# Kernel tuning notes

Hardware: AMD Instinct MI355X
Metric: run time of the kernel (lower is better)

Reference implementation:

```python
import jax, jax.numpy as jnp
import numpy as np

HID = 1024
VOCAB = 50257
MAXLEN = 2048


def setup_inputs() -> dict:
    key = jax.random.key(0)
    ks = jax.random.split(key, 12)
    s = 0.02
    return {
        "input_tok": jax.random.randint(ks[0], (1,), 0, VOCAB),
        "hidden": jax.random.normal(ks[1], (1, 1, HID), jnp.float32),
        "encoder_outputs": jax.random.normal(ks[2], (MAXLEN, HID), jnp.float32),
        "emb": jax.random.normal(ks[3], (VOCAB, HID), jnp.float32) * s,
        "attn_W": jax.random.normal(ks[4], (MAXLEN, 2 * HID), jnp.float32) * s,
        "attn_b": jnp.zeros((MAXLEN,), jnp.float32),
        "comb_W": jax.random.normal(ks[5], (HID, 2 * HID), jnp.float32) * s,
        "comb_b": jnp.zeros((HID,), jnp.float32),
        "W_ih": jax.random.normal(ks[6], (3 * HID, HID), jnp.float32) * s,
        "W_hh": jax.random.normal(ks[7], (3 * HID, HID), jnp.float32) * s,
        "b_ih": jnp.zeros((3 * HID,), jnp.float32),
        "b_hh": jnp.zeros((3 * HID,), jnp.float32),
        "out_W": jax.random.normal(ks[8], (VOCAB, HID), jnp.float32) * s,
        "out_b": jnp.zeros((VOCAB,), jnp.float32),
    }


def reference(input_tok, hidden, encoder_outputs, emb, attn_W, attn_b,
              comb_W, comb_b, W_ih, W_hh, b_ih, b_hh, out_W, out_b):
    H = hidden.shape[-1]
    # embedding lookup -> [1, H]; dropout is identity in eval mode
    embedded = emb[input_tok].reshape(1, H)
    h = hidden[0]  # [1, H]
    # Bahdanau-style attention over fixed max_length
    attn_weights = jax.nn.softmax(
        jnp.concatenate([embedded, h], axis=1) @ attn_W.T + attn_b, axis=1)  # [1, L]
    attn_applied = attn_weights @ encoder_outputs  # [1, H]
    x = jnp.concatenate([embedded, attn_applied], axis=1) @ comb_W.T + comb_b
    x = jax.nn.relu(x)  # [1, H]
    # single GRU step (PyTorch gate layout: r, z, n)
    gi = x @ W_ih.T + b_ih
    gh = h @ W_hh.T + b_hh
    gi_r, gi_z, gi_n = jnp.split(gi, 3, axis=1)
    gh_r, gh_z, gh_n = jnp.split(gh, 3, axis=1)
    r = jax.nn.sigmoid(gi_r + gh_r)
    z = jax.nn.sigmoid(gi_z + gh_z)
    n = jnp.tanh(gi_n + r * gh_n)
    h_new = (1.0 - z) * n + z * h  # [1, H]
    out = jax.nn.log_softmax(h_new @ out_W.T + out_b, axis=1)  # [1, V]
    return out, h_new[None], attn_weights
```

## Files before the change

### kernel.cpp

```cpp
#include <hip/hip_runtime.h>
#include <math.h>

#define HID    1024
#define VOCAB  50257
#define MAXLEN 2048
#define SMB 256
#define SMR (MAXLEN / SMB)
#define LROWS 16
#define LBLK ((VOCAB + LROWS - 1) / LROWS)

#define WS_SCORES    0
#define WS_APPLIED   4096
#define WS_X         5120
#define WS_GI        6144
#define WS_GH        9216
#define WS_HNEW      12288
#define WS_PM        16384
#define WS_PS        30720
#define WS_PARTIALS  49152

__device__ inline float wave_reduce_sum(float v) {
    #pragma unroll
    for (int m = 32; m > 0; m >>= 1) v += __shfl_xor(v, m, 64);
    return v;
}

__global__ __launch_bounds__(256) void k_attn_scores(
        const float* __restrict__ emb, const int* __restrict__ tok,
        const float* __restrict__ hidden,
        const float* __restrict__ attn_W, const float* __restrict__ attn_b,
        float* __restrict__ scores) {
    int gtid = blockIdx.x * blockDim.x + threadIdx.x;
    int row = gtid >> 6, lane = gtid & 63;
    if (row >= MAXLEN) return;
    const float* erow = emb + (size_t)tok[0] * HID;
    const float* wrow = attn_W + (size_t)row * (2 * HID);
    float acc = 0.f;
    #pragma unroll
    for (int i = 0; i < 8; ++i) {
        int k = i * 256 + lane * 4;
        float4 w = *(const float4*)(wrow + k);
        float4 c = (k < HID) ? *(const float4*)(erow + k)
                             : *(const float4*)(hidden + (k - HID));
        acc += w.x * c.x + w.y * c.y + w.z * c.z + w.w * c.w;
    }
    acc = wave_reduce_sum(acc);
    if (lane == 0) scores[row] = acc + attn_b[row];
}

__global__ __launch_bounds__(256) void k_softmax_apply(
        const float* __restrict__ scores, const float* __restrict__ E,
        float* __restrict__ out_w, float* __restrict__ partials) {
    __shared__ float red[256];
    __shared__ float wrow[SMR];
    int t = threadIdx.x, b = blockIdx.x;
    float v[8];
    float m = -INFINITY;
    #pragma unroll
    for (int i = 0; i < 8; ++i) { v[i] = scores[t + 256 * i]; m = fmaxf(m, v[i]); }
    red[t] = m; __syncthreads();
    for (int s = 128; s > 0; s >>= 1) { if (t < s) red[t] = fmaxf(red[t], red[t + s]); __syncthreads(); }
    float M = red[0]; __syncthreads();
    float s = 0.f;
    #pragma unroll
    for (int i = 0; i < 8; ++i) s += expf(v[i] - M);
    red[t] = s; __syncthreads();
    for (int k = 128; k > 0; k >>= 1) { if (t < k) red[t] += red[t + k]; __syncthreads(); }
    float invS = 1.f / red[0];
    int r0 = b * SMR;
    if (t < SMR) wrow[t] = expf(scores[r0 + t] - M) * invS;
    __syncthreads();
    int j = t * 4;
    float4 acc = make_float4(0.f, 0.f, 0.f, 0.f);
    #pragma unroll
    for (int r = 0; r < SMR; ++r) {
        float w = wrow[r];
        float4 e = *(const float4*)(E + (size_t)(r0 + r) * HID + j);
        acc.x += w * e.x; acc.y += w * e.y; acc.z += w * e.z; acc.w += w * e.w;
    }
    *(float4*)(partials + (size_t)b * HID + j) = acc;
    if (b == 0) {
        #pragma unroll
        for (int i = 0; i < 8; ++i) out_w[t + 256 * i] = expf(v[i] - M) * invS;
    }
}

__global__ __launch_bounds__(256) void k_apply_reduce(
        const float* __restrict__ partials, float* __restrict__ applied) {
    __shared__ float sm[4];
    int t = threadIdx.x, j = blockIdx.x;
    float v = partials[(size_t)t * HID + j];
    v = wave_reduce_sum(v);
    int wib = t >> 6, lane = t & 63;
    if (lane == 0) sm[wib] = v;
    __syncthreads();
    if (t == 0) applied[j] = sm[0] + sm[1] + sm[2] + sm[3];
}

__global__ __launch_bounds__(256) void k_comb(
        const float* __restrict__ emb, const int* __restrict__ tok,
        const float* __restrict__ applied,
        const float* __restrict__ comb_W, const float* __restrict__ comb_b,
        float* __restrict__ x) {
    int gtid = blockIdx.x * blockDim.x + threadIdx.x;
    int row = gtid >> 6, lane = gtid & 63;
    if (row >= HID) return;
    const float* erow = emb + (size_t)tok[0] * HID;
    const float* wrow = comb_W + (size_t)row * (2 * HID);
    float acc = 0.f;
    #pragma unroll
    for (int i = 0; i < 8; ++i) {
        int k = i * 256 + lane * 4;
        float4 w = *(const float4*)(wrow + k);
        float4 c = (k < HID) ? *(const float4*)(erow + k)
                             : *(const float4*)(applied + (k - HID));
        acc += w.x * c.x + w.y * c.y + w.z * c.z + w.w * c.w;
    }
    acc = wave_reduce_sum(acc);
    if (lane == 0) x[row] = fmaxf(acc + comb_b[row], 0.f);
}

__global__ __launch_bounds__(256) void k_gru_gemv(
        const float* __restrict__ W_ih, const float* __restrict__ W_hh,
        const float* __restrict__ b_ih, const float* __restrict__ b_hh,
        const float* __restrict__ x, const float* __restrict__ h,
        float* __restrict__ gi, float* __restrict__ gh) {
    int gtid = blockIdx.x * blockDim.x + threadIdx.x;
    int row = gtid >> 6, lane = gtid & 63;
    if (row >= 6 * HID) return;
    const float* wrow; const float* vec;
    if (row < 3 * HID) { wrow = W_ih + (size_t)row * HID; vec = x; }
    else               { wrow = W_hh + (size_t)(row - 3 * HID) * HID; vec = h; }
    float acc = 0.f;
    #pragma unroll
    for (int i = 0; i < 4; ++i) {
        int k = i * 256 + lane * 4;
        float4 w = *(const float4*)(wrow + k);
        float4 c = *(const float4*)(vec + k);
        acc += w.x * c.x + w.y * c.y + w.z * c.z + w.w * c.w;
    }
    acc = wave_reduce_sum(acc);
    if (lane == 0) {
        if (row < 3 * HID) gi[row] = acc + b_ih[row];
        else               gh[row - 3 * HID] = acc + b_hh[row - 3 * HID];
    }
}

__global__ __launch_bounds__(256) void k_gru_gate(
        const float* __restrict__ gi, const float* __restrict__ gh,
        const float* __restrict__ h,
        float* __restrict__ hnew_out, float* __restrict__ hnew_ws) {
    int i = blockIdx.x * blockDim.x + threadIdx.x;
    float r = 1.f / (1.f + expf(-(gi[i] + gh[i])));
    float z = 1.f / (1.f + expf(-(gi[i + HID] + gh[i + HID])));
    float n = tanhf(gi[i + 2 * HID] + r * gh[i + 2 * HID]);
    float hn = (1.f - z) * n + z * h[i];
    hnew_out[i] = hn;
    hnew_ws[i]  = hn;
}

__global__ __launch_bounds__(512) void k_logits(
        const float* __restrict__ hnew, const float* __restrict__ out_W,
        const float* __restrict__ out_b,
        float* __restrict__ logits, float* __restrict__ pm, float* __restrict__ ps) {
    __shared__ float wm[8], wsum[8];
    int wib = threadIdx.x >> 6, lane = threadIdx.x & 63;
    int r0 = blockIdx.x * LROWS + wib * 2;
    bool v0 = r0 < VOCAB, v1 = (r0 + 1) < VOCAB;
    int rr0 = v0 ? r0 : 0, rr1 = v1 ? (r0 + 1) : 0;
    const float* w0 = out_W + (size_t)rr0 * HID;
    const float* w1 = out_W + (size_t)rr1 * HID;
    float acc0 = 0.f, acc1 = 0.f;
    #pragma unroll
    for (int i = 0; i < 4; ++i) {
        int k = i * 256 + lane * 4;
        float4 a = *(const float4*)(w0 + k);
        float4 b = *(const float4*)(w1 + k);
        float4 c = *(const float4*)(hnew + k);
        acc0 += a.x * c.x + a.y * c.y + a.z * c.z + a.w * c.w;
        acc1 += b.x * c.x + b.y * c.y + b.z * c.z + b.w * c.w;
    }
    acc0 = wave_reduce_sum(acc0);
    acc1 = wave_reduce_sum(acc1);
    if (lane == 0) {
        float l0 = acc0 + out_b[rr0], l1 = acc1 + out_b[rr1];
        if (v0) logits[r0] = l0;
        if (v1) logits[r0 + 1] = l1;
        float m, s;
        if (v0 | v1) {
            float e0 = v0 ? l0 : -INFINITY, e1 = v1 ? l1 : -INFINITY;
            m = fmaxf(e0, e1);
            s = (v0 ? expf(e0 - m) : 0.f) + (v1 ? expf(e1 - m) : 0.f);
        } else { m = -INFINITY; s = 0.f; }
        wm[wib] = m; wsum[wib] = s;
    }
    __syncthreads();
    if (threadIdx.x == 0) {
        float M = wm[0];
        #pragma unroll
        for (int i = 1; i < 8; ++i) M = fmaxf(M, wm[i]);
        float S = 0.f;
        #pragma unroll
        for (int i = 0; i < 8; ++i) S += (wsum[i] > 0.f) ? wsum[i] * expf(wm[i] - M) : 0.f;
        pm[blockIdx.x] = M;
        ps[blockIdx.x] = S;
    }
}

__global__ __launch_bounds__(256) void k_logsoftmax_write(
        const float* __restrict__ pm, const float* __restrict__ ps,
        float* __restrict__ out) {
    __shared__ float red[256];
    int t = threadIdx.x;
    float m = -INFINITY;
    for (int i = t; i < LBLK; i += 256) m = fmaxf(m, pm[i]);
    red[t] = m; __syncthreads();
    for (int s = 128; s > 0; s >>= 1) { if (t < s) red[t] = fmaxf(red[t], red[t + s]); __syncthreads(); }
    float M = red[0]; __syncthreads();
    float acc = 0.f;
    for (int i = t; i < LBLK; i += 256) acc += ps[i] * expf(pm[i] - M);
    red[t] = acc; __syncthreads();
    for (int s = 128; s > 0; s >>= 1) { if (t < s) red[t] += red[t + s]; __syncthreads(); }
    float lse = M + logf(red[0]);
    int v = blockIdx.x * 256 + t;
    if (v < VOCAB) out[v] -= lse;
}

extern "C" void kernel_launch(void* const* d_in, const int* in_sizes, int n_in,
                              void* d_out, int out_size, void* d_ws, size_t ws_size,
                              hipStream_t stream) {
    const int*   tok     = (const int*)d_in[0];
    const float* hidden  = (const float*)d_in[1];
    const float* E       = (const float*)d_in[2];
    const float* emb     = (const float*)d_in[3];
    const float* attn_W  = (const float*)d_in[4];
    const float* attn_b  = (const float*)d_in[5];
    const float* comb_W  = (const float*)d_in[6];
    const float* comb_b  = (const float*)d_in[7];
    const float* W_ih    = (const float*)d_in[8];
    const float* W_hh    = (const float*)d_in[9];
    const float* b_ih    = (const float*)d_in[10];
    const float* b_hh    = (const float*)d_in[11];
    const float* out_W   = (const float*)d_in[12];
    const float* out_b   = (const float*)d_in[13];

    float* out       = (float*)d_out;
    float* hnew_out  = out + VOCAB;
    float* attnw_out = out + VOCAB + HID;

    float* ws        = (float*)d_ws;
    float* scores    = ws + WS_SCORES;
    float* applied   = ws + WS_APPLIED;
    float* x         = ws + WS_X;
    float* gi        = ws + WS_GI;
    float* gh        = ws + WS_GH;
    float* hnew_ws   = ws + WS_HNEW;
    float* pm        = ws + WS_PM;
    float* ps        = ws + WS_PS;
    float* partials  = ws + WS_PARTIALS;

    k_attn_scores<<<MAXLEN / 4, 256, 0, stream>>>(emb, tok, hidden, attn_W, attn_b, scores);
    k_softmax_apply<<<SMB, 256, 0, stream>>>(scores, E, attnw_out, partials);
    k_apply_reduce<<<HID, 256, 0, stream>>>(partials, applied);
    k_comb<<<HID / 4, 256, 0, stream>>>(emb, tok, applied, comb_W, comb_b, x);
    k_gru_gemv<<<(6 * HID) / 4, 256, 0, stream>>>(W_ih, W_hh, b_ih, b_hh, x, hidden, gi, gh);
    k_gru_gate<<<HID / 256, 256, 0, stream>>>(gi, gh, hidden, hnew_out, hnew_ws);
    k_logits<<<LBLK, 512, 0, stream>>>(hnew_ws, out_W, out_b, out, pm, ps);
    k_logsoftmax_write<<<(VOCAB + 255) / 256, 256, 0, stream>>>(pm, ps, out);
}
```

Before: 69.27 us.

## Hoist W_hh GEMV into attention kernel, fuse GRU gates, widen logits rows

Result: no change. 70.17 us (+1.3%).

```diff
diff --git a/kernel.cpp b/kernel.cpp
--- a/kernel.cpp
+++ b/kernel.cpp
@@ -6,18 +6,17 @@
 #define MAXLEN 2048
 #define SMB 256
 #define SMR (MAXLEN / SMB)
-#define LROWS 16
+#define LROWS 32
 #define LBLK ((VOCAB + LROWS - 1) / LROWS)
 
 #define WS_SCORES    0
 #define WS_APPLIED   4096
 #define WS_X         5120
-#define WS_GI        6144
-#define WS_GH        9216
+#define WS_GH        6144
 #define WS_HNEW      12288
 #define WS_PM        16384
-#define WS_PS        30720
-#define WS_PARTIALS  49152
+#define WS_PS        20480
+#define WS_PARTIALS  32768
 
 __device__ inline float wave_reduce_sum(float v) {
     #pragma unroll
@@ -25,27 +24,42 @@
     return v;
 }
 
-__global__ __launch_bounds__(256) void k_attn_scores(
+__global__ __launch_bounds__(256) void k_scores_gh(
         const float* __restrict__ emb, const int* __restrict__ tok,
         const float* __restrict__ hidden,
         const float* __restrict__ attn_W, const float* __restrict__ attn_b,
-        float* __restrict__ scores) {
-    int gtid = blockIdx.x * blockDim.x + threadIdx.x;
-    int row = gtid >> 6, lane = gtid & 63;
-    if (row >= MAXLEN) return;
-    const float* erow = emb + (size_t)tok[0] * HID;
-    const float* wrow = attn_W + (size_t)row * (2 * HID);
-    float acc = 0.f;
-    #pragma unroll
-    for (int i = 0; i < 8; ++i) {
-        int k = i * 256 + lane * 4;
-        float4 w = *(const float4*)(wrow + k);
-        float4 c = (k < HID) ? *(const float4*)(erow + k)
-                             : *(const float4*)(hidden + (k - HID));
-        acc += w.x * c.x + w.y * c.y + w.z * c.z + w.w * c.w;
-    }
-    acc = wave_reduce_sum(acc);
-    if (lane == 0) scores[row] = acc + attn_b[row];
+        const float* __restrict__ W_hh, const float* __restrict__ b_hh,
+        float* __restrict__ scores, float* __restrict__ gh) {
+    int wib = threadIdx.x >> 6, lane = threadIdx.x & 63;
+    if (blockIdx.x < 512) {
+        int row = blockIdx.x * 4 + wib;
+        const float* erow = emb + (size_t)tok[0] * HID;
+        const float* wrow = attn_W + (size_t)row * (2 * HID);
+        float acc = 0.f;
+        #pragma unroll
+        for (int i = 0; i < 8; ++i) {
+            int k = i * 256 + lane * 4;
+            float4 w = *(const float4*)(wrow + k);
+            float4 c = (k < HID) ? *(const float4*)(erow + k)
+                                 : *(const float4*)(hidden + (k - HID));
+            acc += w.x * c.x + w.y * c.y + w.z * c.z + w.w * c.w;
+        }
+        acc = wave_reduce_sum(acc);
+        if (lane == 0) scores[row] = acc + attn_b[row];
+    } else {
+        int row = (blockIdx.x - 512) * 4 + wib;
+        const float* wrow = W_hh + (size_t)row * HID;
+        float acc = 0.f;
+        #pragma unroll
+        for (int i = 0; i < 4; ++i) {
+            int k = i * 256 + lane * 4;
+            float4 w = *(const float4*)(wrow + k);
+            float4 c = *(const float4*)(hidden + k);
+            acc += w.x * c.x + w.y * c.y + w.z * c.z + w.w * c.w;
+        }
+        acc = wave_reduce_sum(acc);
+        if (lane == 0) gh[row] = acc + b_hh[row];
+    }
 }
 
 __global__ __launch_bounds__(256) void k_softmax_apply(
@@ -87,14 +101,22 @@
 
 __global__ __launch_bounds__(256) void k_apply_reduce(
         const float* __restrict__ partials, float* __restrict__ applied) {
-    __shared__ float sm[4];
-    int t = threadIdx.x, j = blockIdx.x;
-    float v = partials[(size_t)t * HID + j];
-    v = wave_reduce_sum(v);
-    int wib = t >> 6, lane = t & 63;
-    if (lane == 0) sm[wib] = v;
-    __syncthreads();
-    if (t == 0) applied[j] = sm[0] + sm[1] + sm[2] + sm[3];
+    __shared__ float red[256];
+    int t = threadIdx.x;
+    int co = t & 31, grp = t >> 5;
+    int col = blockIdx.x * 32 + co;
+    float acc = 0.f;
+    #pragma unroll
+    for (int cc = 0; cc < 32; ++cc)
+        acc += partials[(size_t)(grp * 32 + cc) * HID + col];
+    red[grp * 32 + co] = acc;
+    __syncthreads();
+    if (t < 32) {
+        float s = 0.f;
+        #pragma unroll
+        for (int g = 0; g < 8; ++g) s += red[g * 32 + t];
+        applied[blockIdx.x * 32 + t] = s;
+    }
 }
 
 __global__ __launch_bounds__(256) void k_comb(
@@ -120,43 +142,39 @@
     if (lane == 0) x[row] = fmaxf(acc + comb_b[row], 0.f);
 }
 
-__global__ __launch_bounds__(256) void k_gru_gemv(
-        const float* __restrict__ W_ih, const float* __restrict__ W_hh,
-        const float* __restrict__ b_ih, const float* __restrict__ b_hh,
-        const float* __restrict__ x, const float* __restrict__ h,
-        float* __restrict__ gi, float* __restrict__ gh) {
-    int gtid = blockIdx.x * blockDim.x + threadIdx.x;
-    int row = gtid >> 6, lane = gtid & 63;
-    if (row >= 6 * HID) return;
-    const float* wrow; const float* vec;
-    if (row < 3 * HID) { wrow = W_ih + (size_t)row * HID; vec = x; }
-    else               { wrow = W_hh + (size_t)(row - 3 * HID) * HID; vec = h; }
+__global__ __launch_bounds__(384) void k_gru_fused(
+        const float* __restrict__ W_ih, const float* __restrict__ b_ih,
+        const float* __restrict__ x, const float* __restrict__ gh,
+        const float* __restrict__ h,
+        float* __restrict__ hnew_out, float* __restrict__ hnew_ws) {
+    __shared__ float sm[6];
+    int w = threadIdx.x >> 6, lane = threadIdx.x & 63;
+    int hid = blockIdx.x * 2 + (w >= 3 ? 1 : 0);
+    int gate = w % 3;
+    int row = gate * HID + hid;
+    const float* wrow = W_ih + (size_t)row * HID;
     float acc = 0.f;
     #pragma unroll
     for (int i = 0; i < 4; ++i) {
         int k = i * 256 + lane * 4;
-        float4 w = *(const float4*)(wrow + k);
-        float4 c = *(const float4*)(vec + k);
-        acc += w.x * c.x + w.y * c.y + w.z * c.z + w.w * c.w;
+        float4 a = *(const float4*)(wrow + k);
+        float4 c = *(const float4*)(x + k);
+        acc += a.x * c.x + a.y * c.y + a.z * c.z + a.w * c.w;
     }
     acc = wave_reduce_sum(acc);
-    if (lane == 0) {
-        if (row < 3 * HID) gi[row] = acc + b_ih[row];
-        else               gh[row - 3 * HID] = acc + b_hh[row - 3 * HID];
-    }
-}
-
-__global__ __launch_bounds__(256) void k_gru_gate(
-        const float* __restrict__ gi, const float* __restrict__ gh,
-        const float* __restrict__ h,
-        float* __restrict__ hnew_out, float* __restrict__ hnew_ws) {
-    int i = blockIdx.x * blockDim.x + threadIdx.x;
-    float r = 1.f / (1.f + expf(-(gi[i] + gh[i])));
-    float z = 1.f / (1.f + expf(-(gi[i + HID] + gh[i + HID])));
-    float n = tanhf(gi[i + 2 * HID] + r * gh[i + 2 * HID]);
-    float hn = (1.f - z) * n + z * h[i];
-    hnew_out[i] = hn;
-    hnew_ws[i]  = hn;
+    if (lane == 0) sm[w] = acc + b_ih[row];
+    __syncthreads();
+    if (threadIdx.x == 0 || threadIdx.x == 192) {
+        int base = (threadIdx.x == 0) ? 0 : 3;
+        int i = blockIdx.x * 2 + (base ? 1 : 0);
+        float gir = sm[base + 0], giz = sm[base + 1], gin = sm[base + 2];
+        float r = 1.f / (1.f + expf(-(gir + gh[i])));
+        float z = 1.f / (1.f + expf(-(giz + gh[i + HID])));
+        float n = tanhf(gin + r * gh[i + 2 * HID]);
+        float hn = (1.f - z) * n + z * h[i];
+        hnew_out[i] = hn;
+        hnew_ws[i]  = hn;
+    }
 }
 
 __global__ __launch_bounds__(512) void k_logits(
@@ -165,33 +183,37 @@
         float* __restrict__ logits, float* __restrict__ pm, float* __restrict__ ps) {
     __shared__ float wm[8], wsum[8];
     int wib = threadIdx.x >> 6, lane = threadIdx.x & 63;
-    int r0 = blockIdx.x * LROWS + wib * 2;
-    bool v0 = r0 < VOCAB, v1 = (r0 + 1) < VOCAB;
-    int rr0 = v0 ? r0 : 0, rr1 = v1 ? (r0 + 1) : 0;
-    const float* w0 = out_W + (size_t)rr0 * HID;
-    const float* w1 = out_W + (size_t)rr1 * HID;
-    float acc0 = 0.f, acc1 = 0.f;
+    int r0 = blockIdx.x * LROWS + wib * 4;
+    bool val[4]; int rr[4]; const float* wp[4];
+    #pragma unroll
+    for (int j = 0; j < 4; ++j) {
+        val[j] = (r0 + j) < VOCAB;
+        rr[j] = val[j] ? (r0 + j) : 0;
+        wp[j] = out_W + (size_t)rr[j] * HID;
+    }
+    float acc[4] = {0.f, 0.f, 0.f, 0.f};
     #pragma unroll
     for (int i = 0; i < 4; ++i) {
         int k = i * 256 + lane * 4;
-        float4 a = *(const float4*)(w0 + k);
-        float4 b = *(const float4*)(w1 + k);
         float4 c = *(const float4*)(hnew + k);
-        acc0 += a.x * c.x + a.y * c.y + a.z * c.z + a.w * c.w;
-        acc1 += b.x * c.x + b.y * c.y + b.z * c.z + b.w * c.w;
-    }
-    acc0 = wave_reduce_sum(acc0);
-    acc1 = wave_reduce_sum(acc1);
+        #pragma unroll
+        for (int j = 0; j < 4; ++j) {
+            float4 a = *(const float4*)(wp[j] + k);
+            acc[j] += a.x * c.x + a.y * c.y + a.z * c.z + a.w * c.w;
+        }
+    }
+    #pragma unroll
+    for (int j = 0; j < 4; ++j) acc[j] = wave_reduce_sum(acc[j]);
     if (lane == 0) {
-        float l0 = acc0 + out_b[rr0], l1 = acc1 + out_b[rr1];
-        if (v0) logits[r0] = l0;
-        if (v1) logits[r0 + 1] = l1;
-        float m, s;
-        if (v0 | v1) {
-            float e0 = v0 ? l0 : -INFINITY, e1 = v1 ? l1 : -INFINITY;
-            m = fmaxf(e0, e1);
-            s = (v0 ? expf(e0 - m) : 0.f) + (v1 ? expf(e1 - m) : 0.f);
-        } else { m = -INFINITY; s = 0.f; }
+        float l[4], m = -INFINITY;
+        #pragma unroll
+        for (int j = 0; j < 4; ++j) {
+            l[j] = acc[j] + out_b[rr[j]];
+            if (val[j]) { logits[r0 + j] = l[j]; m = fmaxf(m, l[j]); }
+        }
+        float s = 0.f;
+        #pragma unroll
+        for (int j = 0; j < 4; ++j) if (val[j]) s += expf(l[j] - m);
         wm[wib] = m; wsum[wib] = s;
     }
     __syncthreads();
@@ -252,19 +274,18 @@
     float* scores    = ws + WS_SCORES;
     float* applied   = ws + WS_APPLIED;
     float* x         = ws + WS_X;
-    float* gi        = ws + WS_GI;
     float* gh        = ws + WS_GH;
     float* hnew_ws   = ws + WS_HNEW;
     float* pm        = ws + WS_PM;
     float* ps        = ws + WS_PS;
     float* partials  = ws + WS_PARTIALS;
 
-    k_attn_scores<<<MAXLEN / 4, 256, 0, stream>>>(emb, tok, hidden, attn_W, attn_b, scores);
+    k_scores_gh<<<1280, 256, 0, stream>>>(emb, tok, hidden, attn_W, attn_b,
+                                          W_hh, b_hh, scores, gh);
     k_softmax_apply<<<SMB, 256, 0, stream>>>(scores, E, attnw_out, partials);
-    k_apply_reduce<<<HID, 256, 0, stream>>>(partials, applied);
+    k_apply_reduce<<<32, 256, 0, stream>>>(partials, applied);
     k_comb<<<HID / 4, 256, 0, stream>>>(emb, tok, applied, comb_W, comb_b, x);
-    k_gru_gemv<<<(6 * HID) / 4, 256, 0, stream>>>(W_ih, W_hh, b_ih, b_hh, x, hidden, gi, gh);
-    k_gru_gate<<<HID / 256, 256, 0, stream>>>(gi, gh, hidden, hnew_out, hnew_ws);
+    k_gru_fused<<<512, 384, 0, stream>>>(W_ih, b_ih, x, gh, hidden, hnew_out, hnew_ws);
     k_logits<<<LBLK, 512, 0, stream>>>(hnew_ws, out_W, out_b, out, pm, ps);
     k_logsoftmax_write<<<(VOCAB + 255) / 256, 256, 0, stream>>>(pm, ps, out);
 }
```

## Prefetch output projection weights into cache during earlier stages

Applied to the files above, without the earlier changes.

Result: slower. 82.57 us (+19.2%).

```diff
diff --git a/kernel.cpp b/kernel.cpp
--- a/kernel.cpp
+++ b/kernel.cpp
@@ -9,12 +9,18 @@
 #define LROWS 16
 #define LBLK ((VOCAB + LROWS - 1) / LROWS)
 
+#define PF1 128
+#define PF2 64
+#define PF4 64
+#define PF5 112
+
 #define WS_SCORES    0
 #define WS_APPLIED   4096
 #define WS_X         5120
 #define WS_GI        6144
 #define WS_GH        9216
 #define WS_HNEW      12288
+#define WS_PFSINK    14336
 #define WS_PM        16384
 #define WS_PS        30720
 #define WS_PARTIALS  49152
@@ -23,16 +29,34 @@
     #pragma unroll
     for (int m = 32; m > 0; m >>= 1) v += __shfl_xor(v, m, 64);
     return v;
+}
+
+__device__ inline void pf_rows(const float* __restrict__ W, int row0,
+                               float* __restrict__ sink, int sid) {
+    const float4* p = (const float4*)(W + (size_t)row0 * HID);
+    float4 a = make_float4(0.f, 0.f, 0.f, 0.f);
+    #pragma unroll 8
+    for (int r = 0; r < 64; ++r) {
+        float4 v = p[(size_t)r * 256 + threadIdx.x];
+        a.x += v.x; a.y += v.y; a.z += v.z; a.w += v.w;
+    }
+    float s = wave_reduce_sum(a.x + a.y + a.z + a.w);
+    if ((threadIdx.x & 63) == 0) sink[sid * 4 + (threadIdx.x >> 6)] = s;
 }
 
 __global__ __launch_bounds__(256) void k_attn_scores(
         const float* __restrict__ emb, const int* __restrict__ tok,
         const float* __restrict__ hidden,
         const float* __restrict__ attn_W, const float* __restrict__ attn_b,
-        float* __restrict__ scores) {
+        float* __restrict__ scores,
+        const float* __restrict__ out_W, float* __restrict__ sink) {
+    if (blockIdx.x >= 512) {
+        int pfb = blockIdx.x - 512;
+        pf_rows(out_W, pfb * 64, sink, pfb);
+        return;
+    }
     int gtid = blockIdx.x * blockDim.x + threadIdx.x;
     int row = gtid >> 6, lane = gtid & 63;
-    if (row >= MAXLEN) return;
     const float* erow = emb + (size_t)tok[0] * HID;
     const float* wrow = attn_W + (size_t)row * (2 * HID);
     float acc = 0.f;
@@ -50,7 +74,13 @@
 
 __global__ __launch_bounds__(256) void k_softmax_apply(
         const float* __restrict__ scores, const float* __restrict__ E,
-        float* __restrict__ out_w, float* __restrict__ partials) {
+        float* __restrict__ out_w, float* __restrict__ partials,
+        const float* __restrict__ out_W, float* __restrict__ sink) {
+    if (blockIdx.x >= SMB) {
+        int pfb = blockIdx.x - SMB;
+        pf_rows(out_W, 8192 + pfb * 64, sink, PF1 + pfb);
+        return;
+    }
     __shared__ float red[256];
     __shared__ float wrow[SMR];
     int t = threadIdx.x, b = blockIdx.x;
@@ -101,10 +131,15 @@
         const float* __restrict__ emb, const int* __restrict__ tok,
         const float* __restrict__ applied,
         const float* __restrict__ comb_W, const float* __restrict__ comb_b,
-        float* __restrict__ x) {
+        float* __restrict__ x,
+        const float* __restrict__ out_W, float* __restrict__ sink) {
+    if (blockIdx.x >= 256) {
+        int pfb = blockIdx.x - 256;
+        pf_rows(out_W, 12288 + pfb * 64, sink, PF1 + PF2 + pfb);
+        return;
+    }
     int gtid = blockIdx.x * blockDim.x + threadIdx.x;
     int row = gtid >> 6, lane = gtid & 63;
-    if (row >= HID) return;
     const float* erow = emb + (size_t)tok[0] * HID;
     const float* wrow = comb_W + (size_t)row * (2 * HID);
     float acc = 0.f;
@@ -124,10 +159,15 @@
         const float* __restrict__ W_ih, const float* __restrict__ W_hh,
         const float* __restrict__ b_ih, const float* __restrict__ b_hh,
         const float* __restrict__ x, const float* __restrict__ h,
-        float* __restrict__ gi, float* __restrict__ gh) {
+        float* __restrict__ gi, float* __restrict__ gh,
+        const float* __restrict__ out_W, float* __restrict__ sink) {
+    if (blockIdx.x >= 1536) {
+        int pfb = blockIdx.x - 1536;
+        pf_rows(out_W, 16384 + pfb * 64, sink, PF1 + PF2 + PF4 + pfb);
+        return;
+    }
     int gtid = blockIdx.x * blockDim.x + threadIdx.x;
     int row = gtid >> 6, lane = gtid & 63;
-    if (row >= 6 * HID) return;
     const float* wrow; const float* vec;
     if (row < 3 * HID) { wrow = W_ih + (size_t)row * HID; vec = x; }
     else               { wrow = W_hh + (size_t)(row - 3 * HID) * HID; vec = h; }
@@ -255,15 +295,20 @@
     float* gi        = ws + WS_GI;
     float* gh        = ws + WS_GH;
     float* hnew_ws   = ws + WS_HNEW;
+    float* sink      = ws + WS_PFSINK;
     float* pm        = ws + WS_PM;
     float* ps        = ws + WS_PS;
     float* partials  = ws + WS_PARTIALS;
 
-    k_attn_scores<<<MAXLEN / 4, 256, 0, stream>>>(emb, tok, hidden, attn_W, attn_b, scores);
-    k_softmax_apply<<<SMB, 256, 0, stream>>>(scores, E, attnw_out, partials);
+    k_attn_scores<<<512 + PF1, 256, 0, stream>>>(emb, tok, hidden, attn_W, attn_b,
+                                                 scores, out_W, sink);
+    k_softmax_apply<<<SMB + PF2, 256, 0, stream>>>(scores, E, attnw_out, partials,
+                                                   out_W, sink);
     k_apply_reduce<<<HID, 256, 0, stream>>>(partials, applied);
-    k_comb<<<HID / 4, 256, 0, stream>>>(emb, tok, applied, comb_W, comb_b, x);
-    k_gru_gemv<<<(6 * HID) / 4, 256, 0, stream>>>(W_ih, W_hh, b_ih, b_hh, x, hidden, gi, gh);
+    k_comb<<<256 + PF4, 256, 0, stream>>>(emb, tok, applied, comb_W, comb_b, x,
+                                          out_W, sink);
+    k_gru_gemv<<<1536 + PF5, 256, 0, stream>>>(W_ih, W_hh, b_ih, b_hh, x, hidden,
+                                               gi, gh, out_W, sink);
     k_gru_gate<<<HID / 256, 256, 0, stream>>>(gi, gh, hidden, hnew_out, hnew_ws);
     k_logits<<<LBLK, 512, 0, stream>>>(hnew_ws, out_W, out_b, out, pm, ps);
     k_logsoftmax_write<<<(VOCAB + 255) / 256, 256, 0, stream>>>(pm, ps, out);
```
